# Optimization experiments

Hardware: AMD Instinct MI355X
Metric: run time of the kernel (lower is better)

Reference implementation:

```python
import jax, jax.numpy as jnp
import numpy as np

INV_SQRT2 = 0.7071067811865476  # 1/sqrt(2), haar filter coefficient
LEVEL = 2
EFF = 3          # effective modes per axis: (16 // omega=6) + 1
OUT_C = 64
SUBBANDS = ("aad", "ada", "add", "daa", "dad", "dda", "ddd")


def dwt1(x, axis):
    # Haar analysis along `axis` (even length, periodic => no padding needed).
    x = jnp.moveaxis(x, axis, -1)
    e, o = x[..., ::2], x[..., 1::2]
    a = (e + o) * INV_SQRT2
    d = (e - o) * INV_SQRT2
    return jnp.moveaxis(a, -1, axis), jnp.moveaxis(d, -1, axis)


def idwt1(a, d, axis):
    a = jnp.moveaxis(a, axis, -1)
    d = jnp.moveaxis(d, axis, -1)
    e = (a + d) * INV_SQRT2
    o = (a - d) * INV_SQRT2
    x = jnp.stack([e, o], axis=-1).reshape(e.shape[:-1] + (2 * e.shape[-1],))
    return jnp.moveaxis(x, -1, axis)


def dwt3(x):
    # One level of separable 3D DWT over last 3 axes -> dict of 8 subbands.
    ax, dx = dwt1(x, -3)
    out = {}
    for nx, tx in (("a", ax), ("d", dx)):
        ay, dy = dwt1(tx, -2)
        for ny, ty in (("a", ay), ("d", dy)):
            az, dz = dwt1(ty, -1)
            out[nx + ny + "a"] = az
            out[nx + ny + "d"] = dz
    return out


def idwt3(c):
    aa = idwt1(c["aaa"], c["aad"], -1)
    ad = idwt1(c["ada"], c["add"], -1)
    da = idwt1(c["daa"], c["dad"], -1)
    dd = idwt1(c["dda"], c["ddd"], -1)
    a = idwt1(aa, ad, -2)
    d = idwt1(da, dd, -2)
    return idwt1(a, d, -3)


def spectralconv(waves, w4):
    # waves: [B, Ci, X, Y, Z] real; w4: [4, Ci, Co, m, m, m] complex.
    B, Ci, X, Y, Z = waves.shape
    m = EFF
    xw = jnp.fft.rfftn(waves, axes=(-3, -2, -1))
    out = jnp.zeros((B, OUT_C, X, Y, Z // 2 + 1), dtype=xw.dtype)
    mul = lambda blk, w: jnp.einsum("bixyz,ioxyz->boxyz", blk, w)
    out = out.at[:, :, :m, :m, :m].set(mul(xw[:, :, :m, :m, :m], w4[0]))
    out = out.at[:, :, -m:, :m, :m].set(mul(xw[:, :, -m:, :m, :m], w4[1]))
    out = out.at[:, :, :m, -m:, :m].set(mul(xw[:, :, :m, -m:, :m], w4[2]))
    out = out.at[:, :, -m:, -m:, :m].set(mul(xw[:, :, -m:, -m:, :m], w4[3]))
    return jnp.fft.irfftn(out, s=(X, Y, Z), axes=(-3, -2, -1))


def _forward(x, weights):
    # weights: [8, 4, Ci, Co, m, m, m, 2] real -> complex [8, 4, Ci, Co, m, m, m]
    w = jax.lax.complex(weights[..., 0], weights[..., 1])
    # multi-level wavedec3: details[0] = finest, details[-1] = coarsest
    a = x
    details = []
    for _ in range(LEVEL):
        c = dwt3(a)
        a = c.pop("aaa")
        details.append(c)
    # spectral conv on coarsest approx + 7 coarsest detail subbands
    a = spectralconv(a, w[0])
    coarse = details[-1]
    details[-1] = {k: spectralconv(coarse[k], w[i + 1]) for i, k in enumerate(SUBBANDS)}
    # waverec3
    for c in reversed(details):
        full = dict(c)
        full["aaa"] = a
        a = idwt3(full)
    return a


def setup_inputs() -> dict:
    key = jax.random.key(0)
    kx, kw = jax.random.split(key)
    x = jax.random.normal(kx, (4, 64, 64, 64, 64), dtype=jnp.float32)
    scale = 1.0 / (64 * 64)
    weights = scale * jax.random.uniform(kw, (8, 4, 64, 64, 3, 3, 3, 2), dtype=jnp.float32)
    return {"x": x, "weights": weights}


def reference(x, weights):
    return _forward(x, weights)
```

## Files before the change

kernel.cpp:

```cpp
#include <hip/hip_runtime.h>


typedef float f32x4 __attribute__((ext_vector_type(4)));

__device__ __forceinline__ unsigned short f2bf(float v) {
  unsigned u = __float_as_uint(v);
  u = (u + 0x7FFFu + ((u >> 16) & 1u)) >> 16;
  return (unsigned short)u;
}
__device__ __forceinline__ float bf2f(unsigned short b) {
  return __uint_as_float(((unsigned)b) << 16);
}

__constant__ float C16c[16] = {
  1.0f, 0.92387953251128675f, 0.70710678118654752f, 0.38268343236508977f,
  0.0f, -0.38268343236508977f, -0.70710678118654752f, -0.92387953251128675f,
  -1.0f, -0.92387953251128675f, -0.70710678118654752f, -0.38268343236508977f,
  0.0f, 0.38268343236508977f, 0.70710678118654752f, 0.92387953251128675f
};
__constant__ float S16c[16] = {
  0.0f, 0.38268343236508977f, 0.70710678118654752f, 0.92387953251128675f,
  1.0f, 0.92387953251128675f, 0.70710678118654752f, 0.38268343236508977f,
  0.0f, -0.38268343236508977f, -0.70710678118654752f, -0.92387953251128675f,
  -1.0f, -0.92387953251128675f, -0.70710678118654752f, -0.38268343236508977f
};
__constant__ int KYv[6] = {0, 1, 2, 13, 14, 15};

__global__ __launch_bounds__(256) void k1_front_wtr(const float* __restrict__ x,
                                                    const float2* __restrict__ w2,
                                                    float2* __restrict__ g2,
                                                    unsigned* __restrict__ wtu) {
  __shared__ __align__(16) unsigned char smem[13824];
  unsigned tid = threadIdx.x;
  if (blockIdx.x < 4096u) {
    float* sm = (float*)smem;
    float2* fz = (float2*)(smem + 8704);
    unsigned px = blockIdx.x & 15u;
    unsigned bc = blockIdx.x >> 4;
    const f32x4* xp4 = (const f32x4*)(x + ((size_t)bc << 18)) + (size_t)px * 4096u;
    unsigned z4 = tid & 15u;
#pragma unroll
    for (int q = 0; q < 4; q++) {
      float a00 = 0.f, a01 = 0.f, a10 = 0.f, a11 = 0.f;
#pragma unroll
      for (int i = 0; i < 4; i++) {
        f32x4 v = xp4[i * 1024 + q * 256 + tid];
        float h0 = v.x + v.y, h1 = v.z + v.w;
        a00 += h0; a01 += h1;
        if (i < 2) { a10 += h0; a11 += h1; } else { a10 -= h0; a11 -= h1; }
      }
      float p00 = a00 + __shfl_xor(a00, 16);
      float p01 = a01 + __shfl_xor(a01, 16);
      float p10 = a10 + __shfl_xor(a10, 16);
      float p11 = a11 + __shfl_xor(a11, 16);
      float q00 = __shfl_xor(p00, 32), q01 = __shfl_xor(p01, 32);
      float q10 = __shfl_xor(p10, 32), q11 = __shfl_xor(p11, 32);
      bool hi = (tid >> 5) & 1u;
      float ya0 = p00 + q00, yd0 = hi ? (q00 - p00) : (p00 - q00);
      float ya1 = p01 + q01, yd1 = hi ? (q01 - p01) : (p01 - q01);
      float za0 = p10 + q10, zd0 = hi ? (q10 - p10) : (p10 - q10);
      float za1 = p11 + q11, zd1 = hi ? (q11 - p11) : (p11 - q11);
      if (((tid >> 4) & 3u) == 0u) {
        unsigned py = q * 4 + (tid >> 6);
        float* smp = sm + py * 17u + z4;
        smp[0 * 272] = (ya0 + ya1) * 0.125f;
        smp[1 * 272] = (ya0 - ya1) * 0.125f;
        smp[2 * 272] = (yd0 + yd1) * 0.125f;
        smp[3 * 272] = (yd0 - yd1) * 0.125f;
        smp[4 * 272] = (za0 + za1) * 0.125f;
        smp[5 * 272] = (za0 - za1) * 0.125f;
        smp[6 * 272] = (zd0 + zd1) * 0.125f;
        smp[7 * 272] = (zd0 - zd1) * 0.125f;
      }
    }
    __syncthreads();
    if (tid < 128u) {
      unsigned k = tid >> 4, y = tid & 15u;
      const float* row = sm + k * 272u + y * 17u;
#pragma unroll
      for (int kz = 0; kz < 3; kz++) {
        float re = 0.f, im = 0.f;
#pragma unroll
        for (int nz = 0; nz < 16; nz++) {
          float vv = row[nz];
          int t16 = (kz * nz) & 15;
          re += vv * C16c[t16];
          im -= vv * S16c[t16];
        }
        fz[k * 51u + kz * 17u + y] = make_float2(re, im);
      }
    }
    __syncthreads();
    if (tid < 144u) {
      unsigned k = tid / 18u, r = tid - k * 18u;
      unsigned kyi = r / 3u, kz = r - kyi * 3u;
      int ky = KYv[kyi];
      float re = 0.f, im = 0.f;
#pragma unroll
      for (int ny = 0; ny < 16; ny++) {
        float2 vv = fz[k * 51u + kz * 17u + ny];
        int t16 = (ky * ny) & 15;
        float c = C16c[t16], sn = S16c[t16];
        re += vv.x * c + vv.y * sn;
        im += vv.y * c - vv.x * sn;
      }
      g2[((size_t)tid * 16u + px) * 256u + bc] = make_float2(re, im);
    }
  } else {
    f32x4* lw4 = (f32x4*)smem;
    float2* lw2 = (float2*)smem;
    unsigned wb = blockIdx.x - 4096u;
    unsigned kc = wb >> 6, i = wb & 63u;
    const f32x4* src = (const f32x4*)(w2 + ((size_t)kc * 64u + i) * 1728u);
    for (unsigned t = tid; t < 864u; t += 256u)
      lw4[t] = __builtin_nontemporal_load(src + t);
    __syncthreads();
    unsigned* dst = wtu + (size_t)kc * 110592u + (size_t)i * 64u;
    for (unsigned t = tid; t < 1728u; t += 256u) {
      unsigned f = t >> 6, o = t & 63u;
      float2 v = lw2[o * 27u + f];
      unsigned pk = ((unsigned)f2bf(v.y) << 16) | (unsigned)f2bf(v.x);
      __builtin_nontemporal_store(pk, dst + (size_t)f * 4096u + o);
    }
  }
}

__global__ __launch_bounds__(256) void k2_mix(const unsigned* __restrict__ wtu,
                                              const float2* __restrict__ g2,
                                              float2* __restrict__ oh2) {
  __shared__ float2 inl[256];
  unsigned tid = threadIdx.x;
  unsigned f = blockIdx.x % 27u;
  unsigned kc = blockIdx.x / 27u;
  unsigned k = kc >> 2, corner = kc & 3u;
  unsigned kz = f % 3u, kyl = (f / 3u) % 3u, kxl = f / 9u;
  unsigned kxi = kxl + 3u * (corner & 1u);
  unsigned kyi = kyl + 3u * (corner >> 1);
  unsigned fg = kxi * 18u + kyi * 3u + kz;
  unsigned row = k * 18u + kyi * 3u + kz;
  {
    const float2* gp = g2 + (size_t)row * 4096u + tid;
    int kx = KYv[kxi];
    float re = 0.f, im = 0.f;
#pragma unroll
    for (int nx = 0; nx < 16; nx++) {
      float2 vv = gp[nx * 256];
      int t16 = (kx * nx) & 15;
      float c = C16c[t16], sn = S16c[t16];
      re += vv.x * c + vv.y * sn;
      im += vv.y * c - vv.x * sn;
    }
    inl[tid] = make_float2(re, im);
  }
  __syncthreads();
  unsigned b = tid >> 6, o = tid & 63u;
  const unsigned* wp = wtu + ((size_t)kc * 27u + f) * 4096u + o;
  float2 acc = make_float2(0.f, 0.f);
#pragma unroll 16
  for (unsigned i = 0; i < 64u; i++) {
    float2 a = inl[(b << 6) | i];
    unsigned pk = __builtin_nontemporal_load(wp + (size_t)i * 64u);
    float wr = bf2f((unsigned short)(pk & 0xFFFFu));
    float wi = bf2f((unsigned short)(pk >> 16));
    acc.x += a.x * wr - a.y * wi;
    acc.y += a.x * wi + a.y * wr;
  }
  oh2[((size_t)(b * 64u + o)) * 864u + k * 108u + fg] = acc;
}

__global__ __launch_bounds__(256) void k3_invsynth(const float2* __restrict__ oh2,
                                                   const float* __restrict__ x,
                                                   float* __restrict__ out) {
  __shared__ float2 hh[864];
  __shared__ float2 gx[2][8][18];
  __shared__ float2 uu[2][8][3][16];
  __shared__ float W[2][8][16][16];
  unsigned tid = threadIdx.x;
  unsigned sp = blockIdx.x & 7u;
  unsigned bo = 255u - (blockIdx.x >> 3);
  for (unsigned i = tid; i < 864u; i += 256u)
    hh[i] = oh2[(size_t)bo * 864u + i];
  __syncthreads();
  for (unsigned i = tid; i < 288u; i += 256u) {
    unsigned sl = i / 144u, j = i - sl * 144u;
    unsigned k = j / 18u, r = j - k * 18u;
    unsigned nx = sp * 2u + sl;
    float re = 0.f, im = 0.f;
#pragma unroll
    for (int kxi = 0; kxi < 6; kxi++) {
      float2 v = hh[k * 108u + kxi * 18 + r];
      int t16 = (KYv[kxi] * (int)nx) & 15;
      float c = C16c[t16], sn = S16c[t16];
      re += v.x * c - v.y * sn;
      im += v.x * sn + v.y * c;
    }
    gx[sl][k][r] = make_float2(re, im);
  }
  __syncthreads();
  for (unsigned i = tid; i < 768u; i += 256u) {
    unsigned sl = i / 384u, j = i - sl * 384u;
    unsigned k = j / 48u, rem = j - k * 48u;
    unsigned kz = rem >> 4, ny = rem & 15u;
    float re = 0.f, im = 0.f;
#pragma unroll
    for (int kyi = 0; kyi < 6; kyi++) {
      float2 v = gx[sl][k][kyi * 3 + kz];
      int t16 = (KYv[kyi] * (int)ny) & 15;
      float c = C16c[t16], sn = S16c[t16];
      re += v.x * c - v.y * sn;
      im += v.x * sn + v.y * c;
    }
    uu[sl][k][kz][ny] = make_float2(re, im);
  }
  __syncthreads();
  for (unsigned i = tid; i < 512u; i += 256u) {
    unsigned sl = i >> 8, ny = (i >> 4) & 15u, nz = i & 15u;
    float c1 = C16c[nz], s1 = S16c[nz];
    int t2 = (2 * nz) & 15;
    float c2 = C16c[t2], s2 = S16c[t2];
    float val[8];
#pragma unroll
    for (int k = 0; k < 8; k++) {
      float2 u0 = uu[sl][k][0][ny], u1 = uu[sl][k][1][ny], u2 = uu[sl][k][2][ny];
      val[k] = (u0.x + 2.f * (u1.x * c1 - u1.y * s1) + 2.f * (u2.x * c2 - u2.y * s2)) * (1.f / 4096.f);
    }
#pragma unroll
    for (int st = 1; st < 8; st <<= 1)
#pragma unroll
      for (int i2 = 0; i2 < 8; i2++)
        if (!(i2 & st)) {
          float a = val[i2], b = val[i2 | st];
          val[i2] = a + b;
          val[i2 | st] = a - b;
        }
#pragma unroll
    for (int m = 0; m < 8; m++) W[sl][m][ny][nz] = val[m];
  }
  __syncthreads();
  unsigned w = tid >> 6, l = tid & 63u;
  unsigned z4 = l & 15u, y2 = l >> 4;
  unsigned mmy = ((y2 >> 1) & 1u) << 1;
  const float* xp = x + ((size_t)bo << 18);
  float* op = out + ((size_t)bo << 18);
#pragma unroll
  for (unsigned sl = 0; sl < 2u; ++sl) {
#pragma unroll
    for (unsigned r2 = 0; r2 < 8u; ++r2) {
      unsigned xp2 = r2 & 1u, yg = r2 >> 1;
      unsigned X0 = ((sp * 2u + sl) << 2) + (xp2 << 1);
      unsigned Y = (yg << 4) + (w << 2) + y2;
      size_t off = ((size_t)X0 << 12) + (Y << 6) + (z4 << 2);
      f32x4 v0 = *(const f32x4*)(xp + off);
      f32x4 v1 = *(const f32x4*)(xp + off + 4096u);
      float h0 = v0.x + v0.y + v1.x + v1.y;
      float h1 = v0.z + v0.w + v1.z + v1.w;
      float m0 = (h0 + __shfl_xor(h0, 16)) * 0.125f;
      float m1 = (h1 + __shfl_xor(h1, 16)) * 0.125f;
      unsigned ny = (yg << 2) + w;
      unsigned mm = (xp2 << 2) | mmy;
      float c0 = 0.125f * W[sl][mm][ny][z4] - m0;
      float c1 = 0.125f * W[sl][mm | 1u][ny][z4] - m1;
      v0.x += c0; v0.y += c0; v0.z += c1; v0.w += c1;
      v1.x += c0; v1.y += c0; v1.z += c1; v1.w += c1;
      __builtin_nontemporal_store(v0, (f32x4*)(op + off));
      __builtin_nontemporal_store(v1, (f32x4*)(op + off + 4096u));
    }
  }
}

extern "C" void kernel_launch(void* const* d_in, const int* in_sizes, int n_in,
                              void* d_out, int out_size, void* d_ws, size_t ws_size,
                              hipStream_t stream) {
  const float* x = (const float*)d_in[0];
  const float* w = (const float*)d_in[1];
  float* out = (float*)d_out;

  const size_t G_F2 = 144ull * 4096;
  const size_t WT_U = 32ull * 27 * 4096;
  const size_t OH_F2 = 256ull * 864;
  const size_t G_B = G_F2 * 8, WT_B = WT_U * 4, OH_B = OH_F2 * 8;

  float2 *g2, *oh2;
  unsigned* wtu;
  char* ws = (char*)d_ws;
  if (ws_size >= G_B + WT_B + OH_B) {
    g2 = (float2*)ws;
    wtu = (unsigned*)(ws + G_B);
    oh2 = (float2*)(ws + G_B + WT_B);
  } else {
    g2 = (float2*)d_out;
    wtu = (unsigned*)((char*)d_out + G_B);
    oh2 = (float2*)ws;
  }

  k1_front_wtr<<<6144, 256, 0, stream>>>(x, (const float2*)w, g2, wtu);
  k2_mix<<<864, 256, 0, stream>>>(wtu, g2, oh2);
  k3_invsynth<<<2048, 256, 0, stream>>>(oh2, x, out);
}
```

Baseline: 153.9 us.

## Pipeline three stages across batches with a role-dispatching super kernel

Replaces the three sequential kernels with one super kernel whose blocks pick a role (front analysis, channel mix, inverse synthesis, weight transpose) from block-index ranges. It is launched six times, software-pipelined over the batch dimension, so the forward stage of batch b+1 runs alongside the mix of batch b and the synthesis of batch b-1. The aim is to fill the tail and idle time of the small mix and synthesis stages. The mix stage is now per batch, with a 4-way split of the input-channel reduction combined through shared memory. This adds launches, raises shared memory per block to 31 KB for every role, and changes the g2 layout and the fallback workspace placement in the output tail.

```diff
diff --git a/kernel.cpp b/kernel.cpp
--- a/kernel.cpp
+++ b/kernel.cpp
@@ -26,158 +26,152 @@
 };
 __constant__ int KYv[6] = {0, 1, 2, 13, 14, 15};
 
-__global__ __launch_bounds__(256) void k1_front_wtr(const float* __restrict__ x,
-                                                    const float2* __restrict__ w2,
-                                                    float2* __restrict__ g2,
-                                                    unsigned* __restrict__ wtu) {
-  __shared__ __align__(16) unsigned char smem[13824];
+__device__ __forceinline__ void role_ka(unsigned char* smem, unsigned idx, int b,
+                                        const float* __restrict__ x,
+                                        float2* __restrict__ g2) {
+  float* sm = (float*)smem;
+  float2* fz = (float2*)(smem + 8704);
   unsigned tid = threadIdx.x;
-  if (blockIdx.x < 4096u) {
-    float* sm = (float*)smem;
-    float2* fz = (float2*)(smem + 8704);
-    unsigned px = blockIdx.x & 15u;
-    unsigned bc = blockIdx.x >> 4;
-    const f32x4* xp4 = (const f32x4*)(x + ((size_t)bc << 18)) + (size_t)px * 4096u;
-    unsigned z4 = tid & 15u;
-#pragma unroll
-    for (int q = 0; q < 4; q++) {
-      float a00 = 0.f, a01 = 0.f, a10 = 0.f, a11 = 0.f;
-#pragma unroll
-      for (int i = 0; i < 4; i++) {
-        f32x4 v = xp4[i * 1024 + q * 256 + tid];
-        float h0 = v.x + v.y, h1 = v.z + v.w;
-        a00 += h0; a01 += h1;
-        if (i < 2) { a10 += h0; a11 += h1; } else { a10 -= h0; a11 -= h1; }
+  unsigned px = idx & 15u;
+  unsigned c = idx >> 4;
+  unsigned bc = (unsigned)b * 64u + c;
+  const f32x4* xp4 = (const f32x4*)(x + ((size_t)bc << 18)) + (size_t)px * 4096u;
+  unsigned z4 = tid & 15u;
+#pragma unroll
+  for (int q = 0; q < 4; q++) {
+    float a00 = 0.f, a01 = 0.f, a10 = 0.f, a11 = 0.f;
+#pragma unroll
+    for (int i = 0; i < 4; i++) {
+      f32x4 v = xp4[i * 1024 + q * 256 + tid];
+      float h0 = v.x + v.y, h1 = v.z + v.w;
+      a00 += h0; a01 += h1;
+      if (i < 2) { a10 += h0; a11 += h1; } else { a10 -= h0; a11 -= h1; }
+    }
+    float p00 = a00 + __shfl_xor(a00, 16);
+    float p01 = a01 + __shfl_xor(a01, 16);
+    float p10 = a10 + __shfl_xor(a10, 16);
+    float p11 = a11 + __shfl_xor(a11, 16);
+    float q00 = __shfl_xor(p00, 32), q01 = __shfl_xor(p01, 32);
+    float q10 = __shfl_xor(p10, 32), q11 = __shfl_xor(p11, 32);
+    bool hi = (tid >> 5) & 1u;
+    float ya0 = p00 + q00, yd0 = hi ? (q00 - p00) : (p00 - q00);
+    float ya1 = p01 + q01, yd1 = hi ? (q01 - p01) : (p01 - q01);
+    float za0 = p10 + q10, zd0 = hi ? (q10 - p10) : (p10 - q10);
+    float za1 = p11 + q11, zd1 = hi ? (q11 - p11) : (p11 - q11);
+    if (((tid >> 4) & 3u) == 0u) {
+      unsigned py = q * 4 + (tid >> 6);
+      float* smp = sm + py * 17u + z4;
+      smp[0 * 272] = (ya0 + ya1) * 0.125f;
+      smp[1 * 272] = (ya0 - ya1) * 0.125f;
+      smp[2 * 272] = (yd0 + yd1) * 0.125f;
+      smp[3 * 272] = (yd0 - yd1) * 0.125f;
+      smp[4 * 272] = (za0 + za1) * 0.125f;
+      smp[5 * 272] = (za0 - za1) * 0.125f;
+      smp[6 * 272] = (zd0 + zd1) * 0.125f;
+      smp[7 * 272] = (zd0 - zd1) * 0.125f;
+    }
+  }
+  __syncthreads();
+  if (tid < 128u) {
+    unsigned k = tid >> 4, y = tid & 15u;
+    const float* row = sm + k * 272u + y * 17u;
+#pragma unroll
+    for (int kz = 0; kz < 3; kz++) {
+      float re = 0.f, im = 0.f;
+#pragma unroll
+      for (int nz = 0; nz < 16; nz++) {
+        float vv = row[nz];
+        int t16 = (kz * nz) & 15;
+        re += vv * C16c[t16];
+        im -= vv * S16c[t16];
       }
-      float p00 = a00 + __shfl_xor(a00, 16);
-      float p01 = a01 + __shfl_xor(a01, 16);
-      float p10 = a10 + __shfl_xor(a10, 16);
-      float p11 = a11 + __shfl_xor(a11, 16);
-      float q00 = __shfl_xor(p00, 32), q01 = __shfl_xor(p01, 32);
-      float q10 = __shfl_xor(p10, 32), q11 = __shfl_xor(p11, 32);
-      bool hi = (tid >> 5) & 1u;
-      float ya0 = p00 + q00, yd0 = hi ? (q00 - p00) : (p00 - q00);
-      float ya1 = p01 + q01, yd1 = hi ? (q01 - p01) : (p01 - q01);
-      float za0 = p10 + q10, zd0 = hi ? (q10 - p10) : (p10 - q10);
-      float za1 = p11 + q11, zd1 = hi ? (q11 - p11) : (p11 - q11);
-      if (((tid >> 4) & 3u) == 0u) {
-        unsigned py = q * 4 + (tid >> 6);
-        float* smp = sm + py * 17u + z4;
-        smp[0 * 272] = (ya0 + ya1) * 0.125f;
-        smp[1 * 272] = (ya0 - ya1) * 0.125f;
-        smp[2 * 272] = (yd0 + yd1) * 0.125f;
-        smp[3 * 272] = (yd0 - yd1) * 0.125f;
-        smp[4 * 272] = (za0 + za1) * 0.125f;
-        smp[5 * 272] = (za0 - za1) * 0.125f;
-        smp[6 * 272] = (zd0 + zd1) * 0.125f;
-        smp[7 * 272] = (zd0 - zd1) * 0.125f;
-      }
-    }
-    __syncthreads();
-    if (tid < 128u) {
-      unsigned k = tid >> 4, y = tid & 15u;
-      const float* row = sm + k * 272u + y * 17u;
-#pragma unroll
-      for (int kz = 0; kz < 3; kz++) {
-        float re = 0.f, im = 0.f;
-#pragma unroll
-        for (int nz = 0; nz < 16; nz++) {
-          float vv = row[nz];
-          int t16 = (kz * nz) & 15;
-          re += vv * C16c[t16];
-          im -= vv * S16c[t16];
-        }
-        fz[k * 51u + kz * 17u + y] = make_float2(re, im);
-      }
-    }
-    __syncthreads();
-    if (tid < 144u) {
-      unsigned k = tid / 18u, r = tid - k * 18u;
-      unsigned kyi = r / 3u, kz = r - kyi * 3u;
-      int ky = KYv[kyi];
-      float re = 0.f, im = 0.f;
-#pragma unroll
-      for (int ny = 0; ny < 16; ny++) {
-        float2 vv = fz[k * 51u + kz * 17u + ny];
-        int t16 = (ky * ny) & 15;
-        float c = C16c[t16], sn = S16c[t16];
-        re += vv.x * c + vv.y * sn;
-        im += vv.y * c - vv.x * sn;
-      }
-      g2[((size_t)tid * 16u + px) * 256u + bc] = make_float2(re, im);
-    }
-  } else {
-    f32x4* lw4 = (f32x4*)smem;
-    float2* lw2 = (float2*)smem;
-    unsigned wb = blockIdx.x - 4096u;
-    unsigned kc = wb >> 6, i = wb & 63u;
-    const f32x4* src = (const f32x4*)(w2 + ((size_t)kc * 64u + i) * 1728u);
-    for (unsigned t = tid; t < 864u; t += 256u)
-      lw4[t] = __builtin_nontemporal_load(src + t);
-    __syncthreads();
-    unsigned* dst = wtu + (size_t)kc * 110592u + (size_t)i * 64u;
-    for (unsigned t = tid; t < 1728u; t += 256u) {
-      unsigned f = t >> 6, o = t & 63u;
-      float2 v = lw2[o * 27u + f];
-      unsigned pk = ((unsigned)f2bf(v.y) << 16) | (unsigned)f2bf(v.x);
-      __builtin_nontemporal_store(pk, dst + (size_t)f * 4096u + o);
-    }
-  }
-}
-
-__global__ __launch_bounds__(256) void k2_mix(const unsigned* __restrict__ wtu,
-                                              const float2* __restrict__ g2,
-                                              float2* __restrict__ oh2) {
-  __shared__ float2 inl[256];
+      fz[k * 51u + kz * 17u + y] = make_float2(re, im);
+    }
+  }
+  __syncthreads();
+  if (tid < 144u) {
+    unsigned k = tid / 18u, r = tid - k * 18u;
+    unsigned kyi = r / 3u, kz = r - kyi * 3u;
+    int ky = KYv[kyi];
+    float re = 0.f, im = 0.f;
+#pragma unroll
+    for (int ny = 0; ny < 16; ny++) {
+      float2 vv = fz[k * 51u + kz * 17u + ny];
+      int t16 = (ky * ny) & 15;
+      float cc = C16c[t16], sn = S16c[t16];
+      re += vv.x * cc + vv.y * sn;
+      im += vv.y * cc - vv.x * sn;
+    }
+    g2[(((size_t)b * 144u + tid) * 16u + px) * 64u + c] = make_float2(re, im);
+  }
+}
+
+__device__ __forceinline__ void role_mix(unsigned char* smem, unsigned idx, int b,
+                                         const unsigned* __restrict__ wtu,
+                                         const float2* __restrict__ g2,
+                                         float2* __restrict__ oh2) {
+  float2* inl = (float2*)smem;
+  float2* part = (float2*)(smem + 512);
   unsigned tid = threadIdx.x;
-  unsigned f = blockIdx.x % 27u;
-  unsigned kc = blockIdx.x / 27u;
+  unsigned f = idx % 27u;
+  unsigned kc = idx / 27u;
   unsigned k = kc >> 2, corner = kc & 3u;
   unsigned kz = f % 3u, kyl = (f / 3u) % 3u, kxl = f / 9u;
   unsigned kxi = kxl + 3u * (corner & 1u);
   unsigned kyi = kyl + 3u * (corner >> 1);
   unsigned fg = kxi * 18u + kyi * 3u + kz;
   unsigned row = k * 18u + kyi * 3u + kz;
-  {
-    const float2* gp = g2 + (size_t)row * 4096u + tid;
+  if (tid < 64u) {
+    const float2* gp = g2 + (((size_t)b * 144u + row) * 16u) * 64u + tid;
     int kx = KYv[kxi];
     float re = 0.f, im = 0.f;
 #pragma unroll
     for (int nx = 0; nx < 16; nx++) {
-      float2 vv = gp[nx * 256];
+      float2 vv = gp[nx * 64];
       int t16 = (kx * nx) & 15;
-      float c = C16c[t16], sn = S16c[t16];
-      re += vv.x * c + vv.y * sn;
-      im += vv.y * c - vv.x * sn;
+      float cc = C16c[t16], sn = S16c[t16];
+      re += vv.x * cc + vv.y * sn;
+      im += vv.y * cc - vv.x * sn;
     }
     inl[tid] = make_float2(re, im);
   }
   __syncthreads();
-  unsigned b = tid >> 6, o = tid & 63u;
+  unsigned q = tid >> 6, o = tid & 63u;
   const unsigned* wp = wtu + ((size_t)kc * 27u + f) * 4096u + o;
   float2 acc = make_float2(0.f, 0.f);
 #pragma unroll 16
-  for (unsigned i = 0; i < 64u; i++) {
-    float2 a = inl[(b << 6) | i];
+  for (unsigned i = q * 16u; i < q * 16u + 16u; i++) {
+    float2 a = inl[i];
     unsigned pk = __builtin_nontemporal_load(wp + (size_t)i * 64u);
     float wr = bf2f((unsigned short)(pk & 0xFFFFu));
     float wi = bf2f((unsigned short)(pk >> 16));
     acc.x += a.x * wr - a.y * wi;
     acc.y += a.x * wi + a.y * wr;
   }
-  oh2[((size_t)(b * 64u + o)) * 864u + k * 108u + fg] = acc;
-}
-
-__global__ __launch_bounds__(256) void k3_invsynth(const float2* __restrict__ oh2,
-                                                   const float* __restrict__ x,
-                                                   float* __restrict__ out) {
-  __shared__ float2 hh[864];
-  __shared__ float2 gx[2][8][18];
-  __shared__ float2 uu[2][8][3][16];
-  __shared__ float W[2][8][16][16];
+  part[q * 64u + o] = acc;
+  __syncthreads();
+  if (tid < 64u) {
+    float2 r = part[tid];
+#pragma unroll
+    for (int qq = 1; qq < 4; qq++) {
+      float2 p = part[qq * 64u + tid];
+      r.x += p.x; r.y += p.y;
+    }
+    oh2[((size_t)b * 64u + tid) * 864u + k * 108u + fg] = r;
+  }
+}
+
+__device__ __forceinline__ void role_kb(unsigned char* smem, unsigned idx, int b,
+                                        const float2* __restrict__ oh2,
+                                        const float* __restrict__ x,
+                                        float* __restrict__ out) {
+  float2* hh = (float2*)smem;
+  float2* gx = (float2*)(smem + 6912);
+  float2* uu = (float2*)(smem + 9216);
+  float* W = (float*)(smem + 15360);
   unsigned tid = threadIdx.x;
-  unsigned sp = blockIdx.x & 7u;
-  unsigned bo = 255u - (blockIdx.x >> 3);
+  unsigned sp = idx & 7u;
+  unsigned bo = ((unsigned)b << 6) + (idx >> 3);
   for (unsigned i = tid; i < 864u; i += 256u)
     hh[i] = oh2[(size_t)bo * 864u + i];
   __syncthreads();
@@ -190,11 +184,11 @@
     for (int kxi = 0; kxi < 6; kxi++) {
       float2 v = hh[k * 108u + kxi * 18 + r];
       int t16 = (KYv[kxi] * (int)nx) & 15;
-      float c = C16c[t16], sn = S16c[t16];
-      re += v.x * c - v.y * sn;
-      im += v.x * sn + v.y * c;
-    }
-    gx[sl][k][r] = make_float2(re, im);
+      float cc = C16c[t16], sn = S16c[t16];
+      re += v.x * cc - v.y * sn;
+      im += v.x * sn + v.y * cc;
+    }
+    gx[(sl * 8u + k) * 18u + r] = make_float2(re, im);
   }
   __syncthreads();
   for (unsigned i = tid; i < 768u; i += 256u) {
@@ -204,13 +198,13 @@
     float re = 0.f, im = 0.f;
 #pragma unroll
     for (int kyi = 0; kyi < 6; kyi++) {
-      float2 v = gx[sl][k][kyi * 3 + kz];
+      float2 v = gx[(sl * 8u + k) * 18u + kyi * 3 + kz];
       int t16 = (KYv[kyi] * (int)ny) & 15;
-      float c = C16c[t16], sn = S16c[t16];
-      re += v.x * c - v.y * sn;
-      im += v.x * sn + v.y * c;
-    }
-    uu[sl][k][kz][ny] = make_float2(re, im);
+      float cc = C16c[t16], sn = S16c[t16];
+      re += v.x * cc - v.y * sn;
+      im += v.x * sn + v.y * cc;
+    }
+    uu[((sl * 8u + k) * 3u + kz) * 16u + ny] = make_float2(re, im);
   }
   __syncthreads();
   for (unsigned i = tid; i < 512u; i += 256u) {
@@ -221,7 +215,9 @@
     float val[8];
 #pragma unroll
     for (int k = 0; k < 8; k++) {
-      float2 u0 = uu[sl][k][0][ny], u1 = uu[sl][k][1][ny], u2 = uu[sl][k][2][ny];
+      float2 u0 = uu[((sl * 8u + k) * 3u + 0) * 16u + ny];
+      float2 u1 = uu[((sl * 8u + k) * 3u + 1) * 16u + ny];
+      float2 u2 = uu[((sl * 8u + k) * 3u + 2) * 16u + ny];
       val[k] = (u0.x + 2.f * (u1.x * c1 - u1.y * s1) + 2.f * (u2.x * c2 - u2.y * s2)) * (1.f / 4096.f);
     }
 #pragma unroll
@@ -229,12 +225,12 @@
 #pragma unroll
       for (int i2 = 0; i2 < 8; i2++)
         if (!(i2 & st)) {
-          float a = val[i2], b = val[i2 | st];
-          val[i2] = a + b;
-          val[i2 | st] = a - b;
+          float a = val[i2], bb = val[i2 | st];
+          val[i2] = a + bb;
+          val[i2 | st] = a - bb;
         }
 #pragma unroll
-    for (int m = 0; m < 8; m++) W[sl][m][ny][nz] = val[m];
+    for (int m = 0; m < 8; m++) W[((sl * 8u + m) * 16u + ny) * 16u + nz] = val[m];
   }
   __syncthreads();
   unsigned w = tid >> 6, l = tid & 63u;
@@ -258,8 +254,8 @@
       float m1 = (h1 + __shfl_xor(h1, 16)) * 0.125f;
       unsigned ny = (yg << 2) + w;
       unsigned mm = (xp2 << 2) | mmy;
-      float c0 = 0.125f * W[sl][mm][ny][z4] - m0;
-      float c1 = 0.125f * W[sl][mm | 1u][ny][z4] - m1;
+      float c0 = 0.125f * W[((sl * 8u + mm) * 16u + ny) * 16u + z4] - m0;
+      float c1 = 0.125f * W[((sl * 8u + (mm | 1u)) * 16u + ny) * 16u + z4] - m1;
       v0.x += c0; v0.y += c0; v0.z += c1; v0.w += c1;
       v1.x += c0; v1.y += c0; v1.z += c1; v1.w += c1;
       __builtin_nontemporal_store(v0, (f32x4*)(op + off));
@@ -268,17 +264,52 @@
   }
 }
 
+__device__ __forceinline__ void role_wtr(unsigned char* smem, unsigned idx,
+                                         const float2* __restrict__ w2,
+                                         unsigned* __restrict__ wtu) {
+  f32x4* lw4 = (f32x4*)smem;
+  float2* lw2 = (float2*)smem;
+  unsigned tid = threadIdx.x;
+  unsigned kc = idx >> 6, i = idx & 63u;
+  const f32x4* src = (const f32x4*)(w2 + ((size_t)kc * 64u + i) * 1728u);
+  for (unsigned t = tid; t < 864u; t += 256u)
+    lw4[t] = __builtin_nontemporal_load(src + t);
+  __syncthreads();
+  unsigned* dst = wtu + (size_t)kc * 110592u + (size_t)i * 64u;
+  for (unsigned t = tid; t < 1728u; t += 256u) {
+    unsigned f = t >> 6, o = t & 63u;
+    float2 v = lw2[o * 27u + f];
+    unsigned pk = ((unsigned)f2bf(v.y) << 16) | (unsigned)f2bf(v.x);
+    __builtin_nontemporal_store(pk, dst + (size_t)f * 4096u + o);
+  }
+}
+
+__global__ __launch_bounds__(256) void k_super(
+    const float* __restrict__ x, const float2* __restrict__ w2,
+    float2* __restrict__ g2, unsigned* __restrict__ wtu,
+    float2* __restrict__ oh2, float* __restrict__ out,
+    int nKB, int bKB, int nMix, int bMix, int nKA, int bKA) {
+  __shared__ __align__(16) unsigned char smem[31744];
+  unsigned bid = blockIdx.x;
+  if ((int)bid < nKB) { role_kb(smem, bid, bKB, oh2, x, out); return; }
+  bid -= (unsigned)nKB;
+  if ((int)bid < nMix) { role_mix(smem, bid, bMix, wtu, g2, oh2); return; }
+  bid -= (unsigned)nMix;
+  if ((int)bid < nKA) { role_ka(smem, bid, bKA, x, g2); return; }
+  bid -= (unsigned)nKA;
+  role_wtr(smem, bid, w2, wtu);
+}
+
 extern "C" void kernel_launch(void* const* d_in, const int* in_sizes, int n_in,
                               void* d_out, int out_size, void* d_ws, size_t ws_size,
                               hipStream_t stream) {
   const float* x = (const float*)d_in[0];
-  const float* w = (const float*)d_in[1];
+  const float2* w2 = (const float2*)d_in[1];
   float* out = (float*)d_out;
 
-  const size_t G_F2 = 144ull * 4096;
-  const size_t WT_U = 32ull * 27 * 4096;
-  const size_t OH_F2 = 256ull * 864;
-  const size_t G_B = G_F2 * 8, WT_B = WT_U * 4, OH_B = OH_F2 * 8;
+  const size_t G_B = 4ull * 144 * 16 * 64 * 8;
+  const size_t WT_B = 32ull * 27 * 4096 * 4;
+  const size_t OH_B = 256ull * 864 * 8;
 
   float2 *g2, *oh2;
   unsigned* wtu;
@@ -288,12 +319,17 @@
     wtu = (unsigned*)(ws + G_B);
     oh2 = (float2*)(ws + G_B + WT_B);
   } else {
-    g2 = (float2*)d_out;
-    wtu = (unsigned*)((char*)d_out + G_B);
     oh2 = (float2*)ws;
-  }
-
-  k1_front_wtr<<<6144, 256, 0, stream>>>(x, (const float2*)w, g2, wtu);
-  k2_mix<<<864, 256, 0, stream>>>(wtu, g2, oh2);
-  k3_invsynth<<<2048, 256, 0, stream>>>(oh2, x, out);
-}
+    char* tail = (char*)d_out + (size_t)out_size * 4 - (G_B + WT_B);
+    g2 = (float2*)tail;
+    wtu = (unsigned*)(tail + G_B);
+  }
+
+  const int nKA = 1024, nMix = 864, nKB = 512, nWtr = 2048;
+  k_super<<<nKA + nWtr, 256, 0, stream>>>(x, w2, g2, wtu, oh2, out, 0, 0, 0, 0, nKA, 0);
+  k_super<<<nMix + nKA, 256, 0, stream>>>(x, w2, g2, wtu, oh2, out, 0, 0, nMix, 0, nKA, 1);
+  k_super<<<nKB + nMix + nKA, 256, 0, stream>>>(x, w2, g2, wtu, oh2, out, nKB, 0, nMix, 1, nKA, 2);
+  k_super<<<nKB + nMix + nKA, 256, 0, stream>>>(x, w2, g2, wtu, oh2, out, nKB, 1, nMix, 2, nKA, 3);
+  k_super<<<nKB + nMix, 256, 0, stream>>>(x, w2, g2, wtu, oh2, out, nKB, 2, nMix, 3, 0, 0);
+  k_super<<<nKB, 256, 0, stream>>>(x, w2, g2, wtu, oh2, out, nKB, 3, 0, 0, 0, 0);
+}
```

Measured after the change: 179.7 us. 1.17x slower.
